# Optimization experiments

Hardware: AMD Instinct MI355X
Metric: run time of the kernel (lower is better)

Reference implementation:

```python
import jax, jax.numpy as jnp
import numpy as np

B, T, C = 4, 2048, 2048  # batch, n_target, n_context
KEY_SIZE = 1024
VALUE_SIZE = 1024
NUM_HEADS = 16
KEY_HIDDEN = 64
HEAD_SIZE = VALUE_SIZE // NUM_HEADS  # 64
NORMALISE = True


def setup_inputs() -> dict:
    key = jax.random.key(0)
    ks = jax.random.split(key, 7)
    s = 0.02
    return {
        "queries": jax.random.normal(ks[0], (B, T, KEY_SIZE), jnp.float32),
        "keys": jax.random.normal(ks[1], (B, C, KEY_SIZE), jnp.float32),
        "values": jax.random.normal(ks[2], (B, C, VALUE_SIZE), jnp.float32),
        "Wq": jax.random.normal(ks[3], (NUM_HEADS * KEY_HIDDEN, KEY_SIZE), jnp.float32) * s,
        "Wk": jax.random.normal(ks[4], (NUM_HEADS * KEY_HIDDEN, KEY_SIZE), jnp.float32) * s,
        "Wv": jax.random.normal(ks[5], (NUM_HEADS * HEAD_SIZE, VALUE_SIZE), jnp.float32) * s,
        "Wo": jax.random.normal(ks[6], (VALUE_SIZE, NUM_HEADS * HEAD_SIZE), jnp.float32) * s,
    }


def reference(queries, keys, values, Wq, Wk, Wv, Wo):
    # Linear projections (torch nn.Linear: x @ W.T), reshape to heads
    q = (queries @ Wq.T).reshape(B, T, NUM_HEADS, KEY_HIDDEN)   # [B,T,H,Dk]
    k = (keys @ Wk.T).reshape(B, C, NUM_HEADS, KEY_HIDDEN)      # [B,C,H,Dk]
    v = (values @ Wv.T).reshape(B, C, NUM_HEADS, HEAD_SIZE)     # [B,C,H,Dv]
    scale = np.sqrt(KEY_HIDDEN).astype(np.float32)
    # Scores [B,H,T,C]
    scores = jnp.einsum('bthd,bchd->bhtc', q, k) / scale
    if NORMALISE:
        attn = jax.nn.softmax(scores, axis=-1)
    else:
        attn = jax.nn.sigmoid(scores)
    out = jnp.einsum('bhtc,bchd->bthd', attn, v)                # [B,T,H,Dv]
    out = out.reshape(B, T, NUM_HEADS * HEAD_SIZE)
    return out @ Wo.T                                            # [B,T,VALUE_SIZE]
```

## Files before the change

kernel.cpp:

```cpp
#include <hip/hip_runtime.h>
#include <stdint.h>

#define BATCH 4
#define SEQ   2048
#define EMB   1024
#define NH    16
#define HD    64

typedef __attribute__((ext_vector_type(4))) float  floatx4;
typedef __attribute__((ext_vector_type(8))) short  shortx8;

__device__ __forceinline__ unsigned short f2bf(float f) {
  unsigned u = __builtin_bit_cast(unsigned, f);
  u += 0x7FFFu + ((u >> 16) & 1u);
  return (unsigned short)(u >> 16);
}

__device__ __forceinline__ unsigned pack2bf(float a, float b) {
  return (unsigned)f2bf(a) | ((unsigned)f2bf(b) << 16);
}

__device__ __forceinline__ unsigned packtrunc(float a, float b) {
#if __has_builtin(__builtin_amdgcn_perm)
  return __builtin_amdgcn_perm(__builtin_bit_cast(unsigned, b),
                               __builtin_bit_cast(unsigned, a), 0x07060302u);
#else
  return (__builtin_bit_cast(unsigned, a) >> 16) |
         (__builtin_bit_cast(unsigned, b) & 0xFFFF0000u);
#endif
}

__device__ __forceinline__ float fexp2(float x) {
#if __has_builtin(__builtin_amdgcn_exp2f)
  return __builtin_amdgcn_exp2f(x);
#else
  return exp2f(x);
#endif
}

__device__ __forceinline__ void gl_lds16(const void* g, void* l) {
  __builtin_amdgcn_global_load_lds((const __attribute__((address_space(1))) void*)g,
                                   (__attribute__((address_space(3))) void*)l,
                                   16, 0, 0);
}

__device__ __forceinline__ void cast_body(const float* __restrict__ in,
                                          unsigned short* __restrict__ out, int bb, int t) {
  size_t i = (size_t)bb * 256 + t;
  const float4* p = (const float4*)in + i * 2;
  float4 f0 = p[0], f1 = p[1];
  uint4 o;
  o.x = pack2bf(f0.x, f0.y);
  o.y = pack2bf(f0.z, f0.w);
  o.z = pack2bf(f1.x, f1.y);
  o.w = pack2bf(f1.z, f1.w);
  ((uint4*)out)[i] = o;
}

__global__ __launch_bounds__(256) void cast_w4(const float* __restrict__ i0, const float* __restrict__ i1,
                                               const float* __restrict__ i2, const float* __restrict__ i3,
                                               unsigned short* __restrict__ o0, unsigned short* __restrict__ o1,
                                               unsigned short* __restrict__ o2, unsigned short* __restrict__ o3) {
  int bb = blockIdx.x;
  const float* in; unsigned short* out;
  if      (bb < 512)  { in = i0; out = o0; }
  else if (bb < 1024) { in = i1; out = o1; bb -= 512; }
  else if (bb < 1536) { in = i2; out = o2; bb -= 1024; }
  else                { in = i3; out = o3; bb -= 1536; }
  cast_body(in, out, bb, threadIdx.x);
}

#define TST 136
template <int MODE, bool CASTA>
__device__ __forceinline__ void gemm_body(const void* __restrict__ Ap,
                                          const unsigned short* __restrict__ Bt,
                                          void* __restrict__ Cp, float cscale,
                                          unsigned short* As, unsigned short* Bs,
                                          unsigned short* Ts) {
  constexpr int N = EMB, K = EMB;
  constexpr int BM = 128, BN = 128, BK = 64;
  const int t = threadIdx.x, w = t >> 6, lane = t & 63;
  const int quad = lane >> 4, lrow = lane & 15;
  const int m0 = blockIdx.y * BM, n0 = blockIdx.x * BN;
  const int wm = (w >> 1) * 64, wn = (w & 1) * 64;
  floatx4 acc[4][4] = {};

  const unsigned short* asrc[4];
  const float*          afsrc[4];
  int                   adst[4];
  const unsigned short* bsrc[4];
#pragma unroll
  for (int i = 0; i < 4; i++) {
    int q = i * 256 + t;
    int r = q >> 3, kc0 = q & 7, kc = kc0 ^ (r & 7);
    if constexpr (CASTA) {
      afsrc[i] = (const float*)Ap + (size_t)(m0 + r) * K + kc0 * 8;
      adst[i] = r * 64 + kc * 8;
    } else {
      asrc[i] = (const unsigned short*)Ap + (size_t)(m0 + r) * K + kc * 8;
    }
    bsrc[i] = Bt + (size_t)(n0 + r) * K + kc * 8;
  }

  for (int k0 = 0; k0 < K; k0 += BK) {
    if constexpr (CASTA) {
      float4 fa[4][2];
#pragma unroll
      for (int i = 0; i < 4; i++) {
        const float4* s = (const float4*)afsrc[i];
        fa[i][0] = s[0];
        fa[i][1] = s[1];
        afsrc[i] += BK;
      }
#pragma unroll
      for (int i = 0; i < 4; i++) {
        gl_lds16(bsrc[i], (char*)Bs + (size_t)(i * 256 + w * 64) * 16);
        bsrc[i] += BK;
      }
#pragma unroll
      for (int i = 0; i < 4; i++) {
        uint4 o;
        o.x = pack2bf(fa[i][0].x, fa[i][0].y);
        o.y = pack2bf(fa[i][0].z, fa[i][0].w);
        o.z = pack2bf(fa[i][1].x, fa[i][1].y);
        o.w = pack2bf(fa[i][1].z, fa[i][1].w);
        *(uint4*)(As + adst[i]) = o;
      }
    } else {
#pragma unroll
      for (int i = 0; i < 4; i++) {
        gl_lds16(asrc[i], (char*)As + (size_t)(i * 256 + w * 64) * 16);
        gl_lds16(bsrc[i], (char*)Bs + (size_t)(i * 256 + w * 64) * 16);
        asrc[i] += BK; bsrc[i] += BK;
      }
    }
    __syncthreads();
#pragma unroll
    for (int ks = 0; ks < 2; ks++) {
      shortx8 a[4];
#pragma unroll
      for (int mi = 0; mi < 4; mi++) {
        int row = wm + mi * 16 + lrow;
        a[mi] = *(const shortx8*)(As + row * 64 + (((ks * 4 + quad) ^ (row & 7)) * 8));
      }
#pragma unroll
      for (int ni = 0; ni < 4; ni++) {
        int rowb = wn + ni * 16 + lrow;
        shortx8 b = *(const shortx8*)(Bs + rowb * 64 + (((ks * 4 + quad) ^ (rowb & 7)) * 8));
#pragma unroll
        for (int mi = 0; mi < 4; mi++)
          acc[mi][ni] = __builtin_amdgcn_mfma_f32_16x16x32_bf16(a[mi], b, acc[mi][ni], 0, 0, 0);
      }
    }
    __syncthreads();
  }

  if constexpr (MODE == 2) {
#pragma unroll
    for (int u = 0; u < 2; u++)
#pragma unroll
      for (int ni = 0; ni < 4; ni++) {
        uint4 p;
        p.x = pack2bf(acc[2 * u][ni][0], acc[2 * u + 1][ni][0]);
        p.y = pack2bf(acc[2 * u][ni][1], acc[2 * u + 1][ni][1]);
        p.z = pack2bf(acc[2 * u][ni][2], acc[2 * u + 1][ni][2]);
        p.w = pack2bf(acc[2 * u][ni][3], acc[2 * u + 1][ni][3]);
        int col = wn + ni * 16 + lrow;
        int cloc = wm + u * 32 + quad * 8;
        *(uint4*)(Ts + col * TST + cloc) = p;
      }
    __syncthreads();
    unsigned short* vTout = (unsigned short*)Cp;
    const int b = m0 >> 11, cbase = m0 & 2047, h0 = n0 >> 6;
#pragma unroll
    for (int i = 0; i < 8; i++) {
      int g = t + 256 * i;
      int hh2 = g >> 10, d = (g >> 4) & 63, a = g & 15;
      uint4 v = *(const uint4*)(Ts + (hh2 * 64 + d) * TST + a * 8);
      *(uint4*)(vTout + ((size_t)((b * NH + h0 + hh2) * HD + d)) * SEQ + cbase + a * 8) = v;
    }
    __syncthreads();
  } else {
#pragma unroll
    for (int mi = 0; mi < 4; mi++)
#pragma unroll
      for (int ni = 0; ni < 4; ni++)
#pragma unroll
        for (int r = 0; r < 4; r++) {
          int row = m0 + wm + mi * 16 + quad * 4 + r;
          int col = n0 + wn + ni * 16 + lrow;
          float v = acc[mi][ni][r] * cscale;
          if constexpr (MODE == 1) ((float*)Cp)[(size_t)row * N + col] = v;
          else                     ((unsigned short*)Cp)[(size_t)row * N + col] = f2bf(v);
        }
  }
}

__global__ __launch_bounds__(256, 2) void gemm_qkf(
    const float* __restrict__ Xq, const float* __restrict__ Xk,
    const unsigned short* __restrict__ Wq, const unsigned short* __restrict__ Wk,
    unsigned short* __restrict__ Oq, unsigned short* __restrict__ Ok, float sq) {
  __shared__ unsigned short As[128 * 64];
  __shared__ unsigned short Bs[128 * 64];
  if (blockIdx.z == 0) gemm_body<0, true>(Xq, Wq, Oq, sq,   As, Bs, nullptr);
  else                 gemm_body<0, true>(Xk, Wk, Ok, 1.0f, As, Bs, nullptr);
}

__global__ __launch_bounds__(256, 2) void gemm_vtf(const float* __restrict__ Xv,
                                                   const unsigned short* __restrict__ Wv,
                                                   unsigned short* __restrict__ vT) {
  __shared__ unsigned short As[128 * 64];
  __shared__ unsigned short Bs[128 * 64];
  __shared__ unsigned short Ts[128 * TST];
  gemm_body<2, true>(Xv, Wv, vT, 1.0f, As, Bs, Ts);
}

__global__ __launch_bounds__(256, 2) void gemm_o(const unsigned short* __restrict__ A,
                                                 const unsigned short* __restrict__ Bt,
                                                 float* __restrict__ C) {
  __shared__ unsigned short As[128 * 64];
  __shared__ unsigned short Bs[128 * 64];
  gemm_body<1, false>(A, Bt, C, 1.0f, As, Bs, nullptr);
}

__global__ __launch_bounds__(256, 2) void flash_attn(const unsigned short* __restrict__ qp,
                                                     const unsigned short* __restrict__ kp,
                                                     const unsigned short* __restrict__ vT,
                                                     unsigned short* __restrict__ ao) {
  __shared__ unsigned short Ks[2][64 * 64];
  __shared__ unsigned short Vts[2][64 * 64];
  __shared__ unsigned short Ps[4][16 * 40];
  const int h = blockIdx.x & (NH - 1), b = blockIdx.x >> 4;
  const int t0 = blockIdx.y * 256;
  const int t = threadIdx.x, w = t >> 6, lane = t & 63;
  const int quad = lane >> 4, lrow = lane & 15;

  shortx8 qfrag[2][4];
#pragma unroll
  for (int kk = 0; kk < 2; kk++)
#pragma unroll
    for (int mi = 0; mi < 4; mi++) {
      int row = w * 64 + mi * 16 + lrow;
      qfrag[kk][mi] = *(const shortx8*)(qp + ((size_t)(b * SEQ + t0 + row)) * EMB +
                                        h * HD + kk * 32 + quad * 8);
    }

  const unsigned short* ksrc[2];
  const unsigned short* vsrc[2];
#pragma unroll
  for (int i = 0; i < 2; i++) {
    int p = i * 256 + t;
    int r = p >> 3, kc = (p & 7) ^ (r & 7);
    ksrc[i] = kp + ((size_t)(b * SEQ + r)) * EMB + h * HD + kc * 8;
    vsrc[i] = vT + ((size_t)((b * NH + h) * HD + r)) * SEQ + kc * 8;
  }

  float l_st[4][4] = {};
  floatx4 accO[4][4] = {};

#pragma unroll
  for (int i = 0; i < 2; i++) {
    gl_lds16(ksrc[i], (char*)Ks[0] + (size_t)(i * 256 + w * 64) * 16);
    gl_lds16(vsrc[i], (char*)Vts[0] + (size_t)(i * 256 + w * 64) * 16);
    ksrc[i] += 64 * EMB;
    vsrc[i] += 64;
  }
  __syncthreads();

  for (int it = 0; it < SEQ / 64; ++it) {
    const int cur = it & 1;
    const unsigned short* Kc = Ks[cur];
    const unsigned short* Vc = Vts[cur];

    if (it + 1 < SEQ / 64) {
#pragma unroll
      for (int i = 0; i < 2; i++) {
        gl_lds16(ksrc[i], (char*)Ks[cur ^ 1] + (size_t)(i * 256 + w * 64) * 16);
        gl_lds16(vsrc[i], (char*)Vts[cur ^ 1] + (size_t)(i * 256 + w * 64) * 16);
        ksrc[i] += 64 * EMB;
        vsrc[i] += 64;
      }
    }

    floatx4 accS[4][4] = {};
    __builtin_amdgcn_s_setprio(1);
#pragma unroll
    for (int kk = 0; kk < 2; kk++) {
      int qk = quad + kk * 4;
#pragma unroll
      for (int ni = 0; ni < 4; ni++) {
        int rowb = ni * 16 + lrow;
        shortx8 bfr = *(const shortx8*)(Kc + rowb * 64 + ((qk ^ (rowb & 7)) * 8));
#pragma unroll
        for (int mi = 0; mi < 4; mi++)
          accS[mi][ni] = __builtin_amdgcn_mfma_f32_16x16x32_bf16(qfrag[kk][mi], bfr, accS[mi][ni], 0, 0, 0);
      }
    }
    __builtin_amdgcn_s_setprio(0);

#pragma unroll
    for (int hh = 0; hh < 2; hh++) {
      shortx8 pafr[4];
#pragma unroll
      for (int mi = 0; mi < 4; mi++) {
#pragma unroll
        for (int r = 0; r < 4; r++) {
          float p0 = fexp2(accS[mi][2 * hh][r]);
          float p1 = fexp2(accS[mi][2 * hh + 1][r]);
          l_st[mi][r] += p0 + p1;
          *(unsigned*)(&Ps[w][(quad * 4 + r) * 40 + lrow * 2]) = packtrunc(p0, p1);
        }
        pafr[mi] = *(const shortx8*)(&Ps[w][lrow * 40 + quad * 8]);
      }
      __builtin_amdgcn_s_setprio(1);
#pragma unroll
      for (int nio = 0; nio < 4; nio++) {
        int d = nio * 16 + lrow;
        shortx8 bfr = *(const shortx8*)(Vc + d * 64 + ((((hh << 2) + quad) ^ (d & 7)) * 8));
#pragma unroll
        for (int mi = 0; mi < 4; mi++)
          accO[mi][nio] = __builtin_amdgcn_mfma_f32_16x16x32_bf16(pafr[mi], bfr, accO[mi][nio], 0, 0, 0);
      }
      __builtin_amdgcn_s_setprio(0);
    }

    __syncthreads();
  }

#pragma unroll
  for (int mi = 0; mi < 4; mi++)
#pragma unroll
    for (int r = 0; r < 4; r++) {
      float l = l_st[mi][r];
      l += __shfl_xor(l, 1);
      l += __shfl_xor(l, 2);
      l += __shfl_xor(l, 4);
      l += __shfl_xor(l, 8);
      float inv = 1.0f / l;
#pragma unroll
      for (int nio = 0; nio < 4; nio++) accO[mi][nio][r] *= inv;
    }
#pragma unroll
  for (int mi = 0; mi < 4; mi++)
#pragma unroll
    for (int nio = 0; nio < 4; nio++)
#pragma unroll
      for (int r = 0; r < 4; r++) {
        int row = t0 + w * 64 + mi * 16 + quad * 4 + r;
        int col = h * HD + nio * 16 + lrow;
        ao[((size_t)(b * SEQ + row)) * EMB + col] = f2bf(accO[mi][nio][r]);
      }
}

extern "C" void kernel_launch(void* const* d_in, const int* in_sizes, int n_in,
                              void* d_out, int out_size, void* d_ws, size_t ws_size,
                              hipStream_t stream) {
  const float* queries = (const float*)d_in[0];
  const float* keys    = (const float*)d_in[1];
  const float* values  = (const float*)d_in[2];
  const float* Wq      = (const float*)d_in[3];
  const float* Wk      = (const float*)d_in[4];
  const float* Wv      = (const float*)d_in[5];
  const float* Wo      = (const float*)d_in[6];

  char* ws = (char*)d_ws;
  const size_t MB = 1ull << 20;
  const float SC2 = 0.125f * 1.44269504088896341f;

  unsigned short* wq_b = (unsigned short*)(ws + 0 * MB);
  unsigned short* wk_b = (unsigned short*)(ws + 2 * MB);
  unsigned short* wv_b = (unsigned short*)(ws + 4 * MB);
  unsigned short* wo_b = (unsigned short*)(ws + 6 * MB);
  unsigned short* ao   = (unsigned short*)(ws + 8 * MB);
  unsigned short* qp   = (unsigned short*)(ws + 24 * MB);
  unsigned short* kp   = (unsigned short*)(ws + 40 * MB);
  unsigned short* vT   = (unsigned short*)(ws + 56 * MB);

  dim3 gg(EMB / 128, (BATCH * SEQ) / 128);
  dim3 fg(NH * BATCH, SEQ / 256);

  cast_w4<<<2048, 256, 0, stream>>>(Wq, Wk, Wv, Wo, wq_b, wk_b, wv_b, wo_b);
  gemm_qkf<<<dim3(gg.x, gg.y, 2), 256, 0, stream>>>(queries, keys, wq_b, wk_b, qp, kp, SC2);
  gemm_vtf<<<gg, 256, 0, stream>>>(values, wv_b, vT);
  flash_attn<<<fg, 256, 0, stream>>>(qp, kp, vT, ao);
  gemm_o<<<gg, 256, 0, stream>>>(ao, wo_b, (float*)d_out);
}
```

Baseline: 361.3 us.

## Prefetch fp32 A tiles, use hardware bf16 pack, remap blocks per XCD

The fp32 A-operand load for the next K-step is issued right after the barrier, so it overlaps the MFMA work of the current step instead of stalling at the top of the loop. The software round-to-nearest bf16 conversion is replaced with the packed v_cvt_pk_bf16_f32 instruction. Block indices are remapped so consecutive blocks dispatched to the same XCD share M rows, aiming for better L2 reuse of the A tiles. New unused kernels (cast_bf16, gemm_b, gemm_vt) are also added. The remap assumes an 8x8 N grid and a specific grid shape, and keeping the prefetched tile in registers raises register pressure.

```diff
diff --git a/kernel.cpp b/kernel.cpp
--- a/kernel.cpp
+++ b/kernel.cpp
@@ -18,6 +18,12 @@
 
 __device__ __forceinline__ unsigned pack2bf(float a, float b) {
   return (unsigned)f2bf(a) | ((unsigned)f2bf(b) << 16);
+}
+
+__device__ __forceinline__ unsigned cvtpk(float lo, float hi) {
+  unsigned r;
+  asm("v_cvt_pk_bf16_f32 %0, %1, %2" : "=v"(r) : "v"(lo), "v"(hi));
+  return r;
 }
 
 __device__ __forceinline__ unsigned packtrunc(float a, float b) {
@@ -57,6 +63,11 @@
   ((uint4*)out)[i] = o;
 }
 
+__global__ __launch_bounds__(256) void cast_bf16(const float* __restrict__ in,
+                                                 unsigned short* __restrict__ out) {
+  cast_body(in, out, blockIdx.x, threadIdx.x);
+}
+
 __global__ __launch_bounds__(256) void cast_w4(const float* __restrict__ i0, const float* __restrict__ i1,
                                                const float* __restrict__ i2, const float* __restrict__ i3,
                                                unsigned short* __restrict__ o0, unsigned short* __restrict__ o1,
@@ -81,7 +92,10 @@
   constexpr int BM = 128, BN = 128, BK = 64;
   const int t = threadIdx.x, w = t >> 6, lane = t & 63;
   const int quad = lane >> 4, lrow = lane & 15;
-  const int m0 = blockIdx.y * BM, n0 = blockIdx.x * BN;
+  const int lid = blockIdx.x + (int)(gridDim.x * blockIdx.y);
+  const int xcd = lid & 7, slot = lid >> 3;
+  const int m0 = (xcd + 8 * (slot >> 3)) * BM;
+  const int n0 = (slot & 7) * BN;
   const int wm = (w >> 1) * 64, wn = (w & 1) * 64;
   floatx4 acc[4][4] = {};
 
@@ -102,29 +116,32 @@
     bsrc[i] = Bt + (size_t)(n0 + r) * K + kc * 8;
   }
 
+  float4 fa[4][2];
+  if constexpr (CASTA) {
+#pragma unroll
+    for (int i = 0; i < 4; i++) {
+      const float4* s = (const float4*)afsrc[i];
+      fa[i][0] = s[0];
+      fa[i][1] = s[1];
+      afsrc[i] += BK;
+    }
+  }
+
   for (int k0 = 0; k0 < K; k0 += BK) {
     if constexpr (CASTA) {
-      float4 fa[4][2];
 #pragma unroll
       for (int i = 0; i < 4; i++) {
-        const float4* s = (const float4*)afsrc[i];
-        fa[i][0] = s[0];
-        fa[i][1] = s[1];
-        afsrc[i] += BK;
+        uint4 o;
+        o.x = cvtpk(fa[i][0].x, fa[i][0].y);
+        o.y = cvtpk(fa[i][0].z, fa[i][0].w);
+        o.z = cvtpk(fa[i][1].x, fa[i][1].y);
+        o.w = cvtpk(fa[i][1].z, fa[i][1].w);
+        *(uint4*)(As + adst[i]) = o;
       }
 #pragma unroll
       for (int i = 0; i < 4; i++) {
         gl_lds16(bsrc[i], (char*)Bs + (size_t)(i * 256 + w * 64) * 16);
         bsrc[i] += BK;
-      }
-#pragma unroll
-      for (int i = 0; i < 4; i++) {
-        uint4 o;
-        o.x = pack2bf(fa[i][0].x, fa[i][0].y);
-        o.y = pack2bf(fa[i][0].z, fa[i][0].w);
-        o.z = pack2bf(fa[i][1].x, fa[i][1].y);
-        o.w = pack2bf(fa[i][1].z, fa[i][1].w);
-        *(uint4*)(As + adst[i]) = o;
       }
     } else {
 #pragma unroll
@@ -135,6 +152,18 @@
       }
     }
     __syncthreads();
+
+    if constexpr (CASTA) {
+      if (k0 + BK < K) {
+#pragma unroll
+        for (int i = 0; i < 4; i++) {
+          const float4* s = (const float4*)afsrc[i];
+          fa[i][0] = s[0];
+          fa[i][1] = s[1];
+          afsrc[i] += BK;
+        }
+      }
+    }
 #pragma unroll
     for (int ks = 0; ks < 2; ks++) {
       shortx8 a[4];
@@ -215,6 +244,21 @@
   gemm_body<2, true>(Xv, Wv, vT, 1.0f, As, Bs, Ts);
 }
 
+__global__ __launch_bounds__(256, 2) void gemm_b(const unsigned short* __restrict__ A,
+                                                 const unsigned short* __restrict__ Bt,
+                                                 unsigned short* __restrict__ C, float sc) {
+  __shared__ unsigned short As[128 * 64];
+  __shared__ unsigned short Bs[128 * 64];
+  gemm_body<0, false>(A, Bt, C, sc, As, Bs, nullptr);
+}
+__global__ __launch_bounds__(256, 2) void gemm_vt(const unsigned short* __restrict__ A,
+                                                  const unsigned short* __restrict__ Bt,
+                                                  unsigned short* __restrict__ C) {
+  __shared__ unsigned short As[128 * 64];
+  __shared__ unsigned short Bs[128 * 64];
+  __shared__ unsigned short Ts[128 * TST];
+  gemm_body<2, false>(A, Bt, C, 1.0f, As, Bs, Ts);
+}
 __global__ __launch_bounds__(256, 2) void gemm_o(const unsigned short* __restrict__ A,
                                                  const unsigned short* __restrict__ Bt,
                                                  float* __restrict__ C) {
```

Result: faster. 321.7 us (-11.0%).
